# Performance work log

Hardware: AMD Instinct MI355X
Metric: run time of the kernel (lower is better)

## Reference

```python
import jax, jax.numpy as jnp
import numpy as np

N_NODES = 50000
N_EDGES = 800000
F_IN, F_MID, F_OUT = 256, 128, 40


def gcn_conv(x, W, b, src, dst, n_nodes):
    # GCNConv (PyG defaults): add self-loops, symmetric normalization,
    # linear transform, scatter-sum to targets, then bias.
    h = x @ W  # [N, F_out]
    loop = jnp.arange(n_nodes, dtype=src.dtype)
    s = jnp.concatenate([src, loop])  # sources incl. self-loops
    d = jnp.concatenate([dst, loop])  # targets incl. self-loops
    deg = jax.ops.segment_sum(jnp.ones_like(d, dtype=h.dtype), d, num_segments=n_nodes)
    dinv = jnp.where(deg > 0, jax.lax.rsqrt(deg), 0.0)
    norm = dinv[s] * dinv[d]  # [E+N]
    msgs = h[s] * norm[:, None]  # [E+N, F_out]
    out = jax.ops.segment_sum(msgs, d, num_segments=n_nodes)
    return out + b


def setup_inputs() -> dict:
    key = jax.random.key(0)
    ks = jax.random.split(key, 8)
    x = jax.random.normal(ks[0], (N_NODES, F_IN), dtype=jnp.float32)
    edge_index = jax.random.randint(ks[1], (2, N_EDGES), 0, N_NODES, dtype=jnp.int64)

    def glorot(k, fin, fout):
        lim = float(np.sqrt(6.0 / (fin + fout)))
        return jax.random.uniform(k, (fin, fout), jnp.float32, -lim, lim)

    return {
        "x": x,
        "edge_index": edge_index,
        "W_in": glorot(ks[2], F_IN, F_MID),
        "b_in": jnp.zeros((F_MID,), jnp.float32),
        "W_mid": glorot(ks[3], F_MID, F_MID),
        "b_mid": jnp.zeros((F_MID,), jnp.float32),
        "W_out": glorot(ks[4], F_MID, F_OUT),
        "b_out": jnp.zeros((F_OUT,), jnp.float32),
    }


def reference(x, edge_index, W_in, b_in, W_mid, b_mid, W_out, b_out):
    src, dst = edge_index[0], edge_index[1]
    n = x.shape[0]
    # conv_in -> relu (dropout is identity in eval mode)
    h = jax.nn.relu(gcn_conv(x, W_in, b_in, src, dst, n))
    # middle GCN layer -> relu
    h = jax.nn.relu(gcn_conv(h, W_mid, b_mid, src, dst, n))
    # conv_out -> log_softmax over classes
    h = gcn_conv(h, W_out, b_out, src, dst, n)
    return jax.nn.log_softmax(h, axis=-1)
```

## Files before the change

kernel.cpp:

```cpp
#include <hip/hip_runtime.h>
#include <hip/hip_bf16.h>
#include <math.h>


#define F_IN  256
#define F_MID 128
#define F_OUT 40
#define PSH   9
#define BCAP2 10240

typedef __attribute__((ext_vector_type(8))) short bf16x8;
typedef __attribute__((ext_vector_type(4))) float f32x4;

union FragU {
    bf16x8 v;
    __hip_bfloat162 h2[4];
    uint4 u;
    unsigned short s[8];
};

__device__ __forceinline__ unsigned int f2bf(float f) {
    unsigned int u = __float_as_uint(f);
    return (u + 0x7fffu + ((u >> 16) & 1u)) >> 16;
}
__device__ __forceinline__ float bf_lo(unsigned int u) { return __uint_as_float(u << 16); }
__device__ __forceinline__ float bf_hi(unsigned int u) { return __uint_as_float(u & 0xffff0000u); }

__device__ __forceinline__ void add_row(float* acc, uint4 u) {
    acc[0] += bf_lo(u.x); acc[1] += bf_hi(u.x);
    acc[2] += bf_lo(u.y); acc[3] += bf_hi(u.y);
    acc[4] += bf_lo(u.z); acc[5] += bf_hi(u.z);
    acc[6] += bf_lo(u.w); acc[7] += bf_hi(u.w);
}

__global__ __launch_bounds__(256) void k_bucket_prep(const int* __restrict__ src,
                                                     const int* __restrict__ dst,
                                                     unsigned int* __restrict__ bkt,
                                                     int* __restrict__ bcur,
                                                     int E, int nbBkt,
                                                     const float* __restrict__ W1,
                                                     const float* __restrict__ W2,
                                                     const float* __restrict__ W3,
                                                     unsigned short* __restrict__ Wp1,
                                                     unsigned short* __restrict__ Wp2,
                                                     unsigned short* __restrict__ Wp3) {
    if (blockIdx.x >= (unsigned)nbBkt) {
        int t = (blockIdx.x - nbBkt) * 256 + threadIdx.x;
        const float* W; unsigned short* Wp; int M, Mp, kc, nn;
        if (t < 4096)      { W = W1; Wp = Wp1; M = 128; Mp = 128; kc = t >> 7; nn = t & 127; }
        else if (t < 6144) { t -= 4096; W = W2; Wp = Wp2; M = 128; Mp = 128; kc = t >> 7; nn = t & 127; }
        else if (t < 6912) { t -= 6144; W = W3; Wp = Wp3; M = 40;  Mp = 48;  kc = t / 48; nn = t % 48; }
        else return;
        FragU o;
#pragma unroll
        for (int j = 0; j < 8; ++j) {
            int k = kc * 8 + j;
            o.s[j] = (nn < M) ? (unsigned short)f2bf(W[k * M + nn]) : 0;
        }
        *(uint4*)&Wp[((size_t)kc * Mp + nn) * 8] = o.u;
        return;
    }
    __shared__ int hist[128], base[128], cur[128];
    const int t = threadIdx.x;
    if (t < 128) { hist[t] = 0; cur[t] = 0; }
    __syncthreads();
    const int e0 = blockIdx.x * 8192;
    unsigned int mye[32];
#pragma unroll
    for (int j = 0; j < 32; ++j) {
        int e = e0 + j * 256 + t;
        if (e < E) {
            mye[j] = ((unsigned int)dst[e] << 16) | (unsigned int)src[e];
            atomicAdd(&hist[mye[j] >> (16 + PSH)], 1);
        } else mye[j] = 0xffffffffu;
    }
    __syncthreads();
    if (t < 128) base[t] = hist[t] ? atomicAdd(&bcur[t], hist[t]) : 0;
    __syncthreads();
#pragma unroll
    for (int j = 0; j < 32; ++j) {
        if (mye[j] != 0xffffffffu) {
            int p = mye[j] >> (16 + PSH);
            int pos = base[p] + atomicAdd(&cur[p], 1);
            if (pos < BCAP2) bkt[(size_t)p * BCAP2 + pos] = mye[j];
        }
    }
}

__global__ __launch_bounds__(256) void k_gemm1_sort(const unsigned int* __restrict__ bkt,
                                                    const int* __restrict__ bcur,
                                                    int* __restrict__ rofs,
                                                    float* __restrict__ dinv,
                                                    unsigned short* __restrict__ csr,
                                                    int nbG, int npart,
                                                    const float* __restrict__ x,
                                                    const unsigned short* __restrict__ Wp1,
                                                    unsigned short* __restrict__ hn, int n) {
    __shared__ int sh[768];
    if (blockIdx.x >= (unsigned)nbG) {
        int* hist = sh;
        int* stmp = sh + 512;
        const int p = blockIdx.x - nbG;
        const int t = threadIdx.x;
        const int d0 = p << PSH;
        const int nd = min(512, n - d0);

        int bv = (t < p) ? bcur[t] : 0;
        bv = bv > BCAP2 ? BCAP2 : bv;
        stmp[t] = bv;
        hist[t] = 0; hist[t + 256] = 0;
        __syncthreads();
#pragma unroll
        for (int off = 128; off; off >>= 1) {
            if (t < off) stmp[t] += stmp[t + off];
            __syncthreads();
        }
        const int base = stmp[0];
        int np = bcur[p]; np = np > BCAP2 ? BCAP2 : np;
        const unsigned int* b = bkt + (size_t)p * BCAP2;

        for (int i0 = t; i0 < np; i0 += 2048) {
            unsigned int ee[8];
#pragma unroll
            for (int j = 0; j < 8; ++j) {
                int idx = i0 + j * 256;
                ee[j] = (idx < np) ? b[idx] : 0xffffffffu;
            }
#pragma unroll
            for (int j = 0; j < 8; ++j)
                if (ee[j] != 0xffffffffu)
                    atomicAdd(&hist[(int)(ee[j] >> 16) - d0], 1);
        }
        __syncthreads();

        const int h0 = hist[2 * t], h1 = hist[2 * t + 1];
        __syncthreads();
        stmp[t] = h0 + h1;
        __syncthreads();
#pragma unroll
        for (int off = 1; off < 256; off <<= 1) {
            int xx = (t >= off) ? stmp[t - off] : 0;
            __syncthreads();
            stmp[t] += xx;
            __syncthreads();
        }
        const int excl = stmp[t] - (h0 + h1);

        hist[2 * t] = excl;
        hist[2 * t + 1] = excl + h0;
        if (2 * t < nd) {
            rofs[d0 + 2 * t] = base + excl;
            dinv[d0 + 2 * t] = rsqrtf((float)(h0 + 1));
        }
        if (2 * t + 1 < nd) {
            rofs[d0 + 2 * t + 1] = base + excl + h0;
            dinv[d0 + 2 * t + 1] = rsqrtf((float)(h1 + 1));
        }
        if (p == npart - 1 && t == 0) rofs[n] = base + np;
        __syncthreads();

        for (int i0 = t; i0 < np; i0 += 2048) {
            unsigned int ee[8];
#pragma unroll
            for (int j = 0; j < 8; ++j) {
                int idx = i0 + j * 256;
                ee[j] = (idx < np) ? b[idx] : 0xffffffffu;
            }
#pragma unroll
            for (int j = 0; j < 8; ++j) {
                if (ee[j] != 0xffffffffu) {
                    int ld = (int)(ee[j] >> 16) - d0;
                    int pos = atomicAdd(&hist[ld], 1);
                    csr[base + pos] = (unsigned short)(ee[j] & 0xffffu);
                }
            }
        }
        return;
    }
    const int t = threadIdx.x;
    const int w = t >> 6, lane = t & 63, sub = lane & 15, q = lane >> 4;
    const int row0 = blockIdx.x * 64 + w * 16;
    const int row = row0 + sub;
    const bool rv = row < n;
    const float* ap = x + (size_t)row * 256;

    float4 xv[16];
    if (rv) {
#pragma unroll
        for (int j = 0; j < 16; ++j)
            xv[j] = *(const float4*)(ap + (j >> 1) * 32 + q * 8 + (j & 1) * 4);
    } else {
#pragma unroll
        for (int j = 0; j < 16; ++j) xv[j] = make_float4(0.f, 0.f, 0.f, 0.f);
    }

    f32x4 acc[8];
#pragma unroll
    for (int cg = 0; cg < 8; ++cg) acc[cg] = (f32x4)0.f;

#pragma unroll
    for (int kk = 0; kk < 8; ++kk) {
        FragU af;
        float4 f0 = xv[2 * kk];
        float4 f1 = xv[2 * kk + 1];
        af.h2[0] = __float22bfloat162_rn(make_float2(f0.x, f0.y));
        af.h2[1] = __float22bfloat162_rn(make_float2(f0.z, f0.w));
        af.h2[2] = __float22bfloat162_rn(make_float2(f1.x, f1.y));
        af.h2[3] = __float22bfloat162_rn(make_float2(f1.z, f1.w));
        const unsigned short* wrow = Wp1 + (size_t)((kk * 4 + q) * 128 + sub) * 8;
#pragma unroll
        for (int cg = 0; cg < 8; ++cg) {
            bf16x8 b = *(const bf16x8*)(wrow + cg * 16 * 8);
            acc[cg] = __builtin_amdgcn_mfma_f32_16x16x32_bf16(b, af.v, acc[cg], 0, 0, 0);
        }
    }
    if (rv) {
#pragma unroll
        for (int cg = 0; cg < 8; ++cg) {
            uint2 pk;
            pk.x = f2bf(acc[cg][0]) | (f2bf(acc[cg][1]) << 16);
            pk.y = f2bf(acc[cg][2]) | (f2bf(acc[cg][3]) << 16);
            *(uint2*)(hn + (size_t)row * 128 + cg * 16 + q * 4) = pk;
        }
    }
}

__global__ __launch_bounds__(256) void k_scale(unsigned short* __restrict__ hn1,
                                               const float* __restrict__ dinv,
                                               unsigned short* __restrict__ hn2,
                                               unsigned short* __restrict__ hn3,
                                               int n) {
    const int nt = n * 16;
    for (int i = blockIdx.x * 256 + threadIdx.x; i < nt; i += gridDim.x * 256) {
        int row = i >> 4;
        float dv = dinv[row];
        uint4 u = *(const uint4*)(hn1 + (size_t)i * 8);
        uint4 o;
        o.x = f2bf(dv * bf_lo(u.x)) | (f2bf(dv * bf_hi(u.x)) << 16);
        o.y = f2bf(dv * bf_lo(u.y)) | (f2bf(dv * bf_hi(u.y)) << 16);
        o.z = f2bf(dv * bf_lo(u.z)) | (f2bf(dv * bf_hi(u.z)) << 16);
        o.w = f2bf(dv * bf_lo(u.w)) | (f2bf(dv * bf_hi(u.w)) << 16);
        *(uint4*)(hn1 + (size_t)i * 8) = o;
    }
    if (blockIdx.x == 0) {
        int t = threadIdx.x;
        uint4 z = make_uint4(0, 0, 0, 0);
        if (t < 16) *(uint4*)(hn1 + (size_t)n * 128 + t * 8) = z;
        else if (t < 32) *(uint4*)(hn2 + (size_t)n * 128 + (t - 16) * 8) = z;
        else if (t < 52) ((unsigned int*)(hn3 + (size_t)n * 40))[t - 32] = 0;
    }
}

template <int MOUT, int MP>
__global__ __launch_bounds__(256) void k_agg_gemm(const unsigned short* __restrict__ hnS,
                                                  const int* __restrict__ rofs,
                                                  const unsigned short* __restrict__ csr,
                                                  const float* __restrict__ dinv,
                                                  const float* __restrict__ bias,
                                                  const unsigned short* __restrict__ Wp,
                                                  unsigned short* __restrict__ hout,
                                                  int n) {
    __shared__ unsigned short arows[16][136];
    const int t = threadIdx.x;
    const int w = t >> 6, lane = t & 63, sub = lane & 15, q = lane >> 4;
    const int v0 = blockIdx.x * 16;
    const int r = w * 4 + q;
    const int node = v0 + r;
    const bool nv = node < n;

    float acc[8];
#pragma unroll
    for (int k = 0; k < 8; ++k) acc[k] = 0.f;

    int e0 = 0, deg = 0;
    if (nv) { e0 = rofs[node]; deg = rofs[node + 1] - e0; }
    const int total = nv ? deg + 1 : 0;
    int ea = (sub < deg) ? (int)csr[e0 + sub] : n;
    int eb = (16 + sub < deg) ? (int)csr[e0 + 16 + sub] : n;
    const int lim = (total < 33) ? total : 33;

    for (int ix0 = 0; ix0 < lim; ix0 += 8) {
        int sA[8];
#pragma unroll
        for (int jj = 0; jj < 8; ++jj) {
            int ix = ix0 + jj;
            int em = (ix - 1) & 15;
            int srcA = __shfl(ea, (lane & 48) + em);
            int srcB = __shfl(eb, (lane & 48) + em);
            int s = (ix - 1 < 16) ? srcA : srcB;
            s = (ix == 0) ? node : s;
            sA[jj] = (ix < lim) ? s : n;
        }
        uint4 u[8];
#pragma unroll
        for (int jj = 0; jj < 8; ++jj)
            u[jj] = *(const uint4*)(hnS + (size_t)sA[jj] * 128 + sub * 8);
#pragma unroll
        for (int jj = 0; jj < 8; ++jj) add_row(acc, u[jj]);
    }
    for (int ix = 33; ix < total; ++ix) {
        int s = (int)csr[e0 + ix - 1];
        uint4 u = *(const uint4*)(hnS + (size_t)s * 128 + sub * 8);
        add_row(acc, u);
    }

    uint4 pk = make_uint4(0, 0, 0, 0);
    if (nv) {
        float dv = dinv[node];
        float4 b0 = *(const float4*)(bias + sub * 8);
        float4 b1 = *(const float4*)(bias + sub * 8 + 4);
        float o0 = fmaxf(dv * acc[0] + b0.x, 0.f);
        float o1 = fmaxf(dv * acc[1] + b0.y, 0.f);
        float o2 = fmaxf(dv * acc[2] + b0.z, 0.f);
        float o3 = fmaxf(dv * acc[3] + b0.w, 0.f);
        float o4 = fmaxf(dv * acc[4] + b1.x, 0.f);
        float o5 = fmaxf(dv * acc[5] + b1.y, 0.f);
        float o6 = fmaxf(dv * acc[6] + b1.z, 0.f);
        float o7 = fmaxf(dv * acc[7] + b1.w, 0.f);
        pk.x = f2bf(o0) | (f2bf(o1) << 16);
        pk.y = f2bf(o2) | (f2bf(o3) << 16);
        pk.z = f2bf(o4) | (f2bf(o5) << 16);
        pk.w = f2bf(o6) | (f2bf(o7) << 16);
    }
    *(uint4*)&arows[r][sub * 8] = pk;
    __syncthreads();

    const int NCG = MP / 16;
    const int NCGW = (MP == 128) ? 2 : 1;
    f32x4 gacc[2];
#pragma unroll
    for (int i = 0; i < 2; ++i) gacc[i] = (f32x4)0.f;

#pragma unroll
    for (int kstep = 0; kstep < 4; ++kstep) {
        FragU af;
        af.u = *(const uint4*)&arows[sub][kstep * 32 + q * 8];
#pragma unroll
        for (int i = 0; i < NCGW; ++i) {
            int cg = w * NCGW + i;
            if (cg < NCG) {
                bf16x8 b = *(const bf16x8*)(Wp + (size_t)((kstep * 4 + q) * MP + cg * 16 + sub) * 8);
                gacc[i] = __builtin_amdgcn_mfma_f32_16x16x32_bf16(b, af.v, gacc[i], 0, 0, 0);
            }
        }
    }
    const int orow = v0 + sub;
    if (orow < n) {
        float dvr = dinv[orow];
#pragma unroll
        for (int i = 0; i < NCGW; ++i) {
            int cg = w * NCGW + i;
            int feat = cg * 16 + q * 4;
            if (cg < NCG && feat < MOUT) {
                uint2 p2;
                p2.x = f2bf(dvr * gacc[i][0]) | (f2bf(dvr * gacc[i][1]) << 16);
                p2.y = f2bf(dvr * gacc[i][2]) | (f2bf(dvr * gacc[i][3]) << 16);
                *(uint2*)(hout + (size_t)orow * MOUT + feat) = p2;
            }
        }
    }
}

__global__ __launch_bounds__(256) void agg40_lsm_bf16(const unsigned short* __restrict__ hnS,
                                                      const int* __restrict__ rofs,
                                                      const unsigned short* __restrict__ csr,
                                                      const float* __restrict__ dinv,
                                                      const float* __restrict__ bias,
                                                      float* __restrict__ out, int n) {
    int wid = (blockIdx.x * 256 + threadIdx.x) >> 6;
    if (wid >= n) return;
    const int v = wid;
    const int lane = threadIdx.x & 63;
    const int h = lane >> 5;
    const int sl = lane & 31;
    const bool act = sl < 20;
    float a0 = 0.f, a1 = 0.f;
    const int e0 = rofs[v];
    const int total = rofs[v + 1] - e0 + 1;

    for (int i0 = 0; i0 < total; i0 += 16) {
        int sA[8];
#pragma unroll
        for (int j = 0; j < 8; ++j) {
            int ix = i0 + h + 2 * j;
            int s = (ix < total) ? ((ix == 0) ? v : (int)csr[e0 + ix - 1]) : n;
            sA[j] = s;
        }
        if (act) {
#pragma unroll
            for (int j = 0; j < 8; ++j) {
                unsigned int u = *(const unsigned int*)(hnS + (size_t)sA[j] * 40 + sl * 2);
                a0 += bf_lo(u);
                a1 += bf_hi(u);
            }
        }
    }
    a0 += __shfl_xor(a0, 32);
    a1 += __shfl_xor(a1, 32);
    float dv = dinv[v];
    float v0 = act ? (dv * a0 + bias[sl * 2])     : -3.402823466e38f;
    float v1 = act ? (dv * a1 + bias[sl * 2 + 1]) : -3.402823466e38f;
    float m = fmaxf(v0, v1);
#pragma unroll
    for (int off = 16; off; off >>= 1) m = fmaxf(m, __shfl_xor(m, off));
    float p = act ? (__expf(v0 - m) + __expf(v1 - m)) : 0.f;
#pragma unroll
    for (int off = 16; off; off >>= 1) p += __shfl_xor(p, off);
    if (h == 0 && act) {
        float ls = __logf(p);
        *(float2*)(out + (size_t)v * 40 + sl * 2) = make_float2(v0 - m - ls, v1 - m - ls);
    }
}


extern "C" void kernel_launch(void* const* d_in, const int* in_sizes, int n_in,
                              void* d_out, int out_size, void* d_ws, size_t ws_size,
                              hipStream_t stream) {
    const float* x     = (const float*)d_in[0];
    const int*   ei    = (const int*)d_in[1];
    const float* W_in  = (const float*)d_in[2];
    const float* b_in  = (const float*)d_in[3];
    const float* W_mid = (const float*)d_in[4];
    const float* b_mid = (const float*)d_in[5];
    const float* W_out = (const float*)d_in[6];
    const float* b_out = (const float*)d_in[7];
    float* out = (float*)d_out;

    const int N = in_sizes[0] / F_IN;
    const int E = in_sizes[1] / 2;
    const int* srcp = ei;
    const int* dstp = ei + E;
    const int npart = (N + (1 << PSH) - 1) >> PSH;

    char* w = (char*)d_ws;
    unsigned short* hn1 = (unsigned short*)w; w += (size_t)(N + 1) * 128 * 2;
    unsigned short* hn2 = (unsigned short*)w; w += (size_t)(N + 1) * 128 * 2;
    unsigned short* hn3 = (unsigned short*)w; w += (size_t)(N + 1) * 40 * 2 + 16;
    float* dinv = (float*)w; w += (size_t)N * 4;
    int* bcur   = (int*)w;   w += 512;
    int* rofs   = (int*)w;   w += (size_t)(N + 1) * 4 + 12;
    unsigned int* bkt = (unsigned int*)w; w += (size_t)npart * BCAP2 * 4;
    unsigned short* csr = (unsigned short*)w; w += (size_t)E * 2 + 128;
    unsigned short* Wp1 = (unsigned short*)((((size_t)w) + 15) & ~(size_t)15); w = (char*)Wp1 + 32 * 128 * 8 * 2;
    unsigned short* Wp2 = (unsigned short*)w; w += 16 * 128 * 8 * 2;
    unsigned short* Wp3 = (unsigned short*)w; w += 16 * 48 * 8 * 2;

    const int nbW = (N * 64 + 255) / 256;
    const int nbG = (N + 63) / 64;
    const int nbF = (N + 15) / 16;
    const int nbBkt = (E + 8191) / 8192;

    hipMemsetAsync(bcur, 0, 512, stream);
    k_bucket_prep<<<nbBkt + 27, 256, 0, stream>>>(srcp, dstp, bkt, bcur, E, nbBkt,
                                                  W_in, W_mid, W_out, Wp1, Wp2, Wp3);
    k_gemm1_sort<<<nbG + npart, 256, 0, stream>>>(bkt, bcur, rofs, dinv, csr,
                                                  nbG, npart, x, Wp1, hn1, N);
    k_scale<<<2048, 256, 0, stream>>>(hn1, dinv, hn2, hn3, N);
    k_agg_gemm<128, 128><<<nbF, 256, 0, stream>>>(hn1, rofs, csr, dinv, b_in, Wp2, hn2, N);
    k_agg_gemm<40, 48><<<nbF, 256, 0, stream>>>(hn2, rofs, csr, dinv, b_mid, Wp3, hn3, N);
    agg40_lsm_bf16<<<nbW, 256, 0, stream>>>(hn3, rofs, csr, dinv, b_out, out, N);
}
```

Measured before the change: 229.8 us.

## Split sort from GEMM1, fuse dinv scaling into GEMM1 epilogue, prefetch x

```diff
diff --git a/kernel.cpp b/kernel.cpp
--- a/kernel.cpp
+++ b/kernel.cpp
@@ -87,96 +87,118 @@
     }
 }
 
-__global__ __launch_bounds__(256) void k_gemm1_sort(const unsigned int* __restrict__ bkt,
-                                                    const int* __restrict__ bcur,
-                                                    int* __restrict__ rofs,
-                                                    float* __restrict__ dinv,
-                                                    unsigned short* __restrict__ csr,
-                                                    int nbG, int npart,
-                                                    const float* __restrict__ x,
-                                                    const unsigned short* __restrict__ Wp1,
-                                                    unsigned short* __restrict__ hn, int n) {
+__global__ __launch_bounds__(256) void k_sort_pref(const unsigned int* __restrict__ bkt,
+                                                   const int* __restrict__ bcur,
+                                                   int* __restrict__ rofs,
+                                                   float* __restrict__ dinv,
+                                                   unsigned short* __restrict__ csr,
+                                                   int npart, int n,
+                                                   const float* __restrict__ x,
+                                                   int nbPref,
+                                                   unsigned short* __restrict__ hn1,
+                                                   unsigned short* __restrict__ hn2,
+                                                   unsigned short* __restrict__ hn3) {
     __shared__ int sh[768];
-    if (blockIdx.x >= (unsigned)nbG) {
-        int* hist = sh;
-        int* stmp = sh + 512;
-        const int p = blockIdx.x - nbG;
-        const int t = threadIdx.x;
-        const int d0 = p << PSH;
-        const int nd = min(512, n - d0);
-
-        int bv = (t < p) ? bcur[t] : 0;
-        bv = bv > BCAP2 ? BCAP2 : bv;
-        stmp[t] = bv;
-        hist[t] = 0; hist[t + 256] = 0;
+    if (blockIdx.x >= (unsigned)npart) {
+        const int b = blockIdx.x - npart;
+        const float4* xp = (const float4*)x;
+        const int total4 = n * 64;
+        for (int i = b * 256 + threadIdx.x; i < total4; i += nbPref * 256) {
+            float4 v = xp[i];
+            asm volatile("" :: "v"(v.x), "v"(v.y), "v"(v.z), "v"(v.w));
+        }
+        return;
+    }
+    int* hist = sh;
+    int* stmp = sh + 512;
+    const int p = blockIdx.x;
+    const int t = threadIdx.x;
+    const int d0 = p << PSH;
+    const int nd = min(512, n - d0);
+
+    if (p == 0) {
+        uint4 z = make_uint4(0, 0, 0, 0);
+        if (t < 16) *(uint4*)(hn1 + (size_t)n * 128 + t * 8) = z;
+        else if (t < 32) *(uint4*)(hn2 + (size_t)n * 128 + (t - 16) * 8) = z;
+        else if (t < 52) ((unsigned int*)(hn3 + (size_t)n * 40))[t - 32] = 0;
+    }
+
+    int bv = (t < p) ? bcur[t] : 0;
+    bv = bv > BCAP2 ? BCAP2 : bv;
+    stmp[t] = bv;
+    hist[t] = 0; hist[t + 256] = 0;
+    __syncthreads();
+#pragma unroll
+    for (int off = 128; off; off >>= 1) {
+        if (t < off) stmp[t] += stmp[t + off];
         __syncthreads();
-#pragma unroll
-        for (int off = 128; off; off >>= 1) {
-            if (t < off) stmp[t] += stmp[t + off];
-            __syncthreads();
-        }
-        const int base = stmp[0];
-        int np = bcur[p]; np = np > BCAP2 ? BCAP2 : np;
-        const unsigned int* b = bkt + (size_t)p * BCAP2;
-
-        for (int i0 = t; i0 < np; i0 += 2048) {
-            unsigned int ee[8];
-#pragma unroll
-            for (int j = 0; j < 8; ++j) {
-                int idx = i0 + j * 256;
-                ee[j] = (idx < np) ? b[idx] : 0xffffffffu;
+    }
+    const int base = stmp[0];
+    int np = bcur[p]; np = np > BCAP2 ? BCAP2 : np;
+    const unsigned int* b = bkt + (size_t)p * BCAP2;
+
+    for (int i0 = t; i0 < np; i0 += 2048) {
+        unsigned int ee[8];
+#pragma unroll
+        for (int j = 0; j < 8; ++j) {
+            int idx = i0 + j * 256;
+            ee[j] = (idx < np) ? b[idx] : 0xffffffffu;
+        }
+#pragma unroll
+        for (int j = 0; j < 8; ++j)
+            if (ee[j] != 0xffffffffu)
+                atomicAdd(&hist[(int)(ee[j] >> 16) - d0], 1);
+    }
+    __syncthreads();
+
+    const int h0 = hist[2 * t], h1 = hist[2 * t + 1];
+    __syncthreads();
+    stmp[t] = h0 + h1;
+    __syncthreads();
+#pragma unroll
+    for (int off = 1; off < 256; off <<= 1) {
+        int xx = (t >= off) ? stmp[t - off] : 0;
+        __syncthreads();
+        stmp[t] += xx;
+        __syncthreads();
+    }
+    const int excl = stmp[t] - (h0 + h1);
+
+    hist[2 * t] = excl;
+    hist[2 * t + 1] = excl + h0;
+    if (2 * t < nd) {
+        rofs[d0 + 2 * t] = base + excl;
+        dinv[d0 + 2 * t] = rsqrtf((float)(h0 + 1));
+    }
+    if (2 * t + 1 < nd) {
+        rofs[d0 + 2 * t + 1] = base + excl + h0;
+        dinv[d0 + 2 * t + 1] = rsqrtf((float)(h1 + 1));
+    }
+    if (p == npart - 1 && t == 0) rofs[n] = base + np;
+    __syncthreads();
+
+    for (int i0 = t; i0 < np; i0 += 2048) {
+        unsigned int ee[8];
+#pragma unroll
+        for (int j = 0; j < 8; ++j) {
+            int idx = i0 + j * 256;
+            ee[j] = (idx < np) ? b[idx] : 0xffffffffu;
+        }
+#pragma unroll
+        for (int j = 0; j < 8; ++j) {
+            if (ee[j] != 0xffffffffu) {
+                int ld = (int)(ee[j] >> 16) - d0;
+                int pos = atomicAdd(&hist[ld], 1);
+                csr[base + pos] = (unsigned short)(ee[j] & 0xffffu);
             }
-#pragma unroll
-            for (int j = 0; j < 8; ++j)
-                if (ee[j] != 0xffffffffu)
-                    atomicAdd(&hist[(int)(ee[j] >> 16) - d0], 1);
-        }
-        __syncthreads();
-
-        const int h0 = hist[2 * t], h1 = hist[2 * t + 1];
-        __syncthreads();
-        stmp[t] = h0 + h1;
-        __syncthreads();
-#pragma unroll
-        for (int off = 1; off < 256; off <<= 1) {
-            int xx = (t >= off) ? stmp[t - off] : 0;
-            __syncthreads();
-            stmp[t] += xx;
-            __syncthreads();
-        }
-        const int excl = stmp[t] - (h0 + h1);
-
-        hist[2 * t] = excl;
-        hist[2 * t + 1] = excl + h0;
-        if (2 * t < nd) {
-            rofs[d0 + 2 * t] = base + excl;
-            dinv[d0 + 2 * t] = rsqrtf((float)(h0 + 1));
-        }
-        if (2 * t + 1 < nd) {
-            rofs[d0 + 2 * t + 1] = base + excl + h0;
-            dinv[d0 + 2 * t + 1] = rsqrtf((float)(h1 + 1));
-        }
-        if (p == npart - 1 && t == 0) rofs[n] = base + np;
-        __syncthreads();
-
-        for (int i0 = t; i0 < np; i0 += 2048) {
-            unsigned int ee[8];
-#pragma unroll
-            for (int j = 0; j < 8; ++j) {
-                int idx = i0 + j * 256;
-                ee[j] = (idx < np) ? b[idx] : 0xffffffffu;
-            }
-#pragma unroll
-            for (int j = 0; j < 8; ++j) {
-                if (ee[j] != 0xffffffffu) {
-                    int ld = (int)(ee[j] >> 16) - d0;
-                    int pos = atomicAdd(&hist[ld], 1);
-                    csr[base + pos] = (unsigned short)(ee[j] & 0xffffu);
-                }
-            }
-        }
-        return;
-    }
+        }
+    }
+}
+
+__global__ __launch_bounds__(256) void k_gemm1s(const float* __restrict__ x,
+                                                const unsigned short* __restrict__ Wp1,
+                                                const float* __restrict__ dinv,
+                                                unsigned short* __restrict__ hn, int n) {
     const int t = threadIdx.x;
     const int w = t >> 6, lane = t & 63, sub = lane & 15, q = lane >> 4;
     const int row0 = blockIdx.x * 64 + w * 16;
@@ -215,39 +237,14 @@
         }
     }
     if (rv) {
+        float dv = dinv[row];
 #pragma unroll
         for (int cg = 0; cg < 8; ++cg) {
             uint2 pk;
-            pk.x = f2bf(acc[cg][0]) | (f2bf(acc[cg][1]) << 16);
-            pk.y = f2bf(acc[cg][2]) | (f2bf(acc[cg][3]) << 16);
+            pk.x = f2bf(dv * acc[cg][0]) | (f2bf(dv * acc[cg][1]) << 16);
+            pk.y = f2bf(dv * acc[cg][2]) | (f2bf(dv * acc[cg][3]) << 16);
             *(uint2*)(hn + (size_t)row * 128 + cg * 16 + q * 4) = pk;
         }
-    }
-}
-
-__global__ __launch_bounds__(256) void k_scale(unsigned short* __restrict__ hn1,
-                                               const float* __restrict__ dinv,
-                                               unsigned short* __restrict__ hn2,
-                                               unsigned short* __restrict__ hn3,
-                                               int n) {
-    const int nt = n * 16;
-    for (int i = blockIdx.x * 256 + threadIdx.x; i < nt; i += gridDim.x * 256) {
-        int row = i >> 4;
-        float dv = dinv[row];
-        uint4 u = *(const uint4*)(hn1 + (size_t)i * 8);
-        uint4 o;
-        o.x = f2bf(dv * bf_lo(u.x)) | (f2bf(dv * bf_hi(u.x)) << 16);
-        o.y = f2bf(dv * bf_lo(u.y)) | (f2bf(dv * bf_hi(u.y)) << 16);
-        o.z = f2bf(dv * bf_lo(u.z)) | (f2bf(dv * bf_hi(u.z)) << 16);
-        o.w = f2bf(dv * bf_lo(u.w)) | (f2bf(dv * bf_hi(u.w)) << 16);
-        *(uint4*)(hn1 + (size_t)i * 8) = o;
-    }
-    if (blockIdx.x == 0) {
-        int t = threadIdx.x;
-        uint4 z = make_uint4(0, 0, 0, 0);
-        if (t < 16) *(uint4*)(hn1 + (size_t)n * 128 + t * 8) = z;
-        else if (t < 32) *(uint4*)(hn2 + (size_t)n * 128 + (t - 16) * 8) = z;
-        else if (t < 52) ((unsigned int*)(hn3 + (size_t)n * 40))[t - 32] = 0;
     }
 }
 
@@ -449,13 +446,14 @@
     const int nbG = (N + 63) / 64;
     const int nbF = (N + 15) / 16;
     const int nbBkt = (E + 8191) / 8192;
+    const int nbPref = 256;
 
     hipMemsetAsync(bcur, 0, 512, stream);
     k_bucket_prep<<<nbBkt + 27, 256, 0, stream>>>(srcp, dstp, bkt, bcur, E, nbBkt,
                                                   W_in, W_mid, W_out, Wp1, Wp2, Wp3);
-    k_gemm1_sort<<<nbG + npart, 256, 0, stream>>>(bkt, bcur, rofs, dinv, csr,
-                                                  nbG, npart, x, Wp1, hn1, N);
-    k_scale<<<2048, 256, 0, stream>>>(hn1, dinv, hn2, hn3, N);
+    k_sort_pref<<<npart + nbPref, 256, 0, stream>>>(bkt, bcur, rofs, dinv, csr,
+                                                    npart, N, x, nbPref, hn1, hn2, hn3);
+    k_gemm1s<<<nbG, 256, 0, stream>>>(x, Wp1, dinv, hn1, N);
     k_agg_gemm<128, 128><<<nbF, 256, 0, stream>>>(hn1, rofs, csr, dinv, b_in, Wp2, hn2, N);
     k_agg_gemm<40, 48><<<nbF, 256, 0, stream>>>(hn2, rofs, csr, dinv, b_mid, Wp3, hn3, N);
     agg40_lsm_bf16<<<nbW, 256, 0, stream>>>(hn3, rofs, csr, dinv, b_out, out, N);
```

Result: slower. 244.6 us (+6.4%).
